# Optimization experiments

Hardware: AMD Instinct MI355X
Metric: run time of the kernel (lower is better)

Reference implementation:

```python
import jax, jax.numpy as jnp
import numpy as np

DIM = 256
NUM_HEADS = 8
KS = 3
DILATIONS = (1, 2, 3, 4)
HEAD_DIM = DIM // NUM_HEADS
SCALE = HEAD_DIM ** -0.5
HIDDEN = 4 * DIM


def setup_inputs() -> dict:
    key = jax.random.key(0)
    ks = jax.random.split(key, 8)
    B, H, W = 4, 64, 64

    def w(k, shape):
        return jax.random.normal(k, shape, jnp.float32) * 0.02

    return {
        "x": jax.random.normal(ks[0], (2, B, DIM, H, W), jnp.float32),
        "norm1_w": jnp.ones((2, DIM), jnp.float32),
        "norm1_b": jnp.zeros((2, DIM), jnp.float32),
        "q_w": w(ks[1], (2, DIM, DIM)),
        "k_w": w(ks[2], (2, DIM, DIM)),
        "v_w": w(ks[3], (2, DIM, DIM)),
        "proj_w": w(ks[4], (2, DIM, DIM)),
        "proj_b": jnp.zeros((2, DIM), jnp.float32),
        "norm2_w": jnp.ones((2, DIM), jnp.float32),
        "norm2_b": jnp.zeros((2, DIM), jnp.float32),
        "fc1_w": w(ks[5], (2, HIDDEN, DIM)),
        "fc1_b": jnp.zeros((2, HIDDEN), jnp.float32),
        "fc2_w": w(ks[6], (2, DIM, HIDDEN)),
        "fc2_b": jnp.zeros((2, DIM), jnp.float32),
    }


def _layer_norm(x, w, b, eps=1e-5):
    mu = jnp.mean(x, -1, keepdims=True)
    var = jnp.mean((x - mu) ** 2, -1, keepdims=True)
    return (x - mu) * jax.lax.rsqrt(var + eps) * w + b


def _unfold(x, ks, dil):
    # x: (B, d, H, W) -> (B, d, ks*ks, H, W); zero-padded dilated local patches
    # matches nn.Unfold(ks, dilation=dil, padding=dil*(ks-1)//2): channel-major,
    # kernel positions row-major inner.
    B, d, H, W = x.shape
    p = dil * (ks - 1) // 2
    xp = jnp.pad(x, ((0, 0), (0, 0), (p, p), (p, p)))
    pats = [xp[:, :, i * dil:i * dil + H, j * dil:j * dil + W]
            for i in range(ks) for j in range(ks)]
    return jnp.stack(pats, axis=2)


def _dilate_attn(q, k, v, dil):
    # q,k,v: (B, d, H, W) with d = DIM // num_dilation
    B, d, H, W = q.shape
    h = d // HEAD_DIM
    N = H * W
    kk = KS * KS
    qh = q.reshape(B, h, HEAD_DIM, N)                        # b h c n
    kp = _unfold(k, KS, dil).reshape(B, h, HEAD_DIM, kk, N)  # b h c k n
    attn = jnp.einsum('bhcn,bhckn->bhnk', qh, kp) * SCALE    # b h n kk
    attn = jax.nn.softmax(attn, axis=-1)
    vp = _unfold(v, KS, dil).reshape(B, h, HEAD_DIM, kk, N)
    out = jnp.einsum('bhnk,bhckn->bhnc', attn, vp)           # b h n c
    return out.transpose(0, 2, 1, 3).reshape(B, H, W, d)     # B H W d


def _mda(x1, x2, x3, qw, kw, vw, pw, pb):
    # MultiDilatelocalAttention; x*: (B, H, W, C)
    nd = len(DILATIONS)
    cd = DIM // nd
    q = jnp.einsum('bhwc,oc->bohw', x1, qw)  # 1x1 conv, no bias
    k = jnp.einsum('bhwc,oc->bohw', x2, kw)
    v = jnp.einsum('bhwc,oc->bohw', x3, vw)
    outs = [_dilate_attn(q[:, i * cd:(i + 1) * cd], k[:, i * cd:(i + 1) * cd],
                         v[:, i * cd:(i + 1) * cd], DILATIONS[i])
            for i in range(nd)]
    x = jnp.concatenate(outs, axis=-1)  # (B, H, W, C)
    return x @ pw.T + pb


def _block(x1, x2, x3, p, bi):
    # DilateBlock; inputs BCHW
    x1, x2, x3 = (t.transpose(0, 2, 3, 1) for t in (x1, x2, x3))
    n1 = lambda t: _layer_norm(t, p['norm1_w'][bi], p['norm1_b'][bi])
    x = x1 + _mda(n1(x1), n1(x2), n1(x3), p['q_w'][bi], p['k_w'][bi],
                  p['v_w'][bi], p['proj_w'][bi], p['proj_b'][bi])
    h = _layer_norm(x, p['norm2_w'][bi], p['norm2_b'][bi])
    h = jax.nn.gelu(h @ p['fc1_w'][bi].T + p['fc1_b'][bi], approximate=False)
    x = x + h @ p['fc2_w'][bi].T + p['fc2_b'][bi]
    return x.transpose(0, 3, 1, 2)


def reference(x, norm1_w, norm1_b, q_w, k_w, v_w, proj_w, proj_b,
              norm2_w, norm2_b, fc1_w, fc1_b, fc2_w, fc2_b):
    p = dict(norm1_w=norm1_w, norm1_b=norm1_b, q_w=q_w, k_w=k_w, v_w=v_w,
             proj_w=proj_w, proj_b=proj_b, norm2_w=norm2_w, norm2_b=norm2_b,
             fc1_w=fc1_w, fc1_b=fc1_b, fc2_w=fc2_w, fc2_b=fc2_b)
    vi, ir = x[0], x[1]
    vi_ir_div = _block(vi - ir, ir, ir, p, 0)
    ir_vi_div = _block(ir - vi, vi, vi, p, 1)
    return (vi_ir_div, ir_vi_div)
```

## Files before the change

### kernel.cpp

```cpp
#include <hip/hip_runtime.h>
#include <hip/hip_bf16.h>

typedef __attribute__((ext_vector_type(8))) short bf16x8;
typedef __attribute__((ext_vector_type(4))) float f32x4;

#define HWSZ 4096
#define NPIX 16384

__device__ inline float b2f(short s) {
  return __uint_as_float(((unsigned)(unsigned short)s) << 16);
}
__device__ inline short f2b(float f) {
  __hip_bfloat16 h = __float2bfloat16(f);
  return *(short*)&h;
}
__device__ inline void gl16(const short* g, short* l) {
  __builtin_amdgcn_global_load_lds(
      (const __attribute__((address_space(1))) unsigned int*)g,
      (__attribute__((address_space(3))) unsigned int*)l, 16, 0, 0);
}
__device__ inline float gelu_f(float x) {
  float ax = fabsf(x) * 0.70710678118654752f;
  float t = 1.f / (1.f + 0.3275911f * ax);
  float y = t * (0.254829592f + t * (-0.284496736f + t * (1.421413741f +
            t * (-1.453152027f + t * 1.061405429f))));
  float erfv = 1.f - y * __expf(-ax * ax);
  erfv = copysignf(erfv, x);
  return 0.5f * x * (1.f + erfv);
}

__global__ __launch_bounds__(256) void convert_k(
    const float* __restrict__ qw, const float* __restrict__ kw,
    const float* __restrict__ vw, const float* __restrict__ pw,
    const float* __restrict__ f1, const float* __restrict__ f2,
    __hip_bfloat16* __restrict__ out)
{
  int idx = blockIdx.x * 256 + threadIdx.x;
  if (idx >= 2 * 786432) return;
  int bi = idx / 786432;
  int r  = idx - bi * 786432;
  float v;
  if      (r <  65536) v = qw[bi*65536 + r];
  else if (r < 131072) v = kw[bi*65536 + r - 65536];
  else if (r < 196608) v = vw[bi*65536 + r - 131072];
  else if (r < 262144) v = pw[bi*65536 + r - 196608];
  else if (r < 524288) v = f1[bi*262144 + r - 262144];
  else                 v = f2[bi*262144 + r - 524288];
  out[idx] = __float2bfloat16(v);
}

__global__ __launch_bounds__(256) void prep2_k(
    const float* __restrict__ x,
    const float* __restrict__ nw, const float* __restrict__ nb,
    __hip_bfloat16* __restrict__ ln1a,
    __hip_bfloat16* __restrict__ ln1b,
    __hip_bfloat16* __restrict__ diff,
    float av, float ai, float bv, float bb)
{
  __shared__ float t1[16][257], t2[16][257];
  __shared__ float red[4][16][16];
  __shared__ float mu1[16], rs1[16], mu2[16], rs2[16];
  int t = threadIdx.x;
  int pix0 = blockIdx.x * 16;
  int b = pix0 >> 12, hw0 = pix0 & 4095;
  const float* vi = x + (size_t)b * 256 * HWSZ;
  const float* ir = x + (size_t)(4 + b) * 256 * HWSZ;

  for (int it = 0; it < 16; ++it) {
    int idx = it * 256 + t;
    int p = idx & 15, c = idx >> 4;
    size_t off = (size_t)c * HWSZ + hw0 + p;
    float a = vi[off], bb2 = ir[off];
    t1[p][c] = av * a + ai * bb2;
    t2[p][c] = bv * a + bb * bb2;
  }
  __syncthreads();
  {
    int p = t & 15, q = t >> 4;
    float s1 = 0, ss1 = 0, s2 = 0, ss2 = 0;
    for (int i = 0; i < 16; ++i) {
      float v = t1[p][q*16 + i]; s1 += v; ss1 += v*v;
      float u = t2[p][q*16 + i]; s2 += u; ss2 += u*u;
    }
    red[0][p][q] = s1; red[1][p][q] = ss1; red[2][p][q] = s2; red[3][p][q] = ss2;
  }
  __syncthreads();
  if (t < 32) {
    int p = t & 15, which = t >> 4;
    float s = 0, ss = 0;
    for (int q = 0; q < 16; ++q) { s += red[which*2][p][q]; ss += red[which*2+1][p][q]; }
    float mu = s * (1.f/256.f);
    float var = ss * (1.f/256.f) - mu*mu;
    float rs = rsqrtf(var + 1e-5f);
    if (which == 0) { mu1[p] = mu; rs1[p] = rs; }
    else            { mu2[p] = mu; rs2[p] = rs; }
  }
  __syncthreads();
  for (int it = 0; it < 16; ++it) {
    float v1 = t1[it][t], v2 = t2[it][t];
    size_t o = (size_t)(pix0 + it) * 256 + t;
    ln1a[o] = __float2bfloat16((v1 - mu1[it]) * rs1[it] * nw[t] + nb[t]);
    ln1b[o] = __float2bfloat16((v2 - mu2[it]) * rs2[it] * nw[t] + nb[t]);
    diff[o] = __float2bfloat16(v1);
  }
}

template<int EPI, int BN>
__device__ __forceinline__ void gemm_core(
    const short* __restrict__ A, const short* __restrict__ W,
    void* __restrict__ outp, const float* __restrict__ bias,
    const short* __restrict__ res, int K, int ldc, int m0, int n0)
{
  constexpr int NI = (BN == 128) ? 4 : 2;
  __shared__ __align__(16) short As[2][64 * 32];
  __shared__ __align__(16) short Bs[2][BN * 32];
  int tid = threadIdx.x;
  int l = tid & 63, wv = tid >> 6;
  int wm = wv >> 1, wn = wv & 1;
  int lr = l & 15, lq = l >> 4;

  int srow = tid >> 2;
  int sch = (tid & 3) ^ ((srow >> 1) & 3);
  const short* gA = A + (size_t)(m0 + srow) * K + sch * 8;
  const short* gB = W + (size_t)(n0 + srow) * K + sch * 8;
  const short* gB1 = (BN == 128) ? (W + (size_t)(n0 + srow + 64) * K + sch * 8) : nullptr;

  f32x4 acc[2][NI];
  #pragma unroll
  for (int mi = 0; mi < 2; ++mi)
    #pragma unroll
    for (int ni = 0; ni < NI; ++ni) acc[mi][ni] = (f32x4){0.f, 0.f, 0.f, 0.f};

  gl16(gA, &As[0][0] + tid * 8);
  gl16(gB, &Bs[0][0] + tid * 8);
  if constexpr (BN == 128) gl16(gB1, &Bs[0][0] + 2048 + tid * 8);
  __syncthreads();

  int cur = 0;
  int rowa0 = wm * 32 + lr;
  int rowb0 = wn * (BN / 2) + lr;
  for (int k0 = 0; k0 < K; k0 += 32) {
    int kn = k0 + 32;
    if (kn < K) {
      gl16(gA + kn, &As[cur ^ 1][0] + tid * 8);
      gl16(gB + kn, &Bs[cur ^ 1][0] + tid * 8);
      if constexpr (BN == 128) gl16(gB1 + kn, &Bs[cur ^ 1][0] + 2048 + tid * 8);
    }
    bf16x8 af[2], bfr[NI];
    #pragma unroll
    for (int mi = 0; mi < 2; ++mi) {
      int row = rowa0 + mi * 16;
      int kc = lq ^ ((row >> 1) & 3);
      af[mi] = *(const bf16x8*)(&As[cur][0] + row * 32 + kc * 8);
    }
    #pragma unroll
    for (int ni = 0; ni < NI; ++ni) {
      int row = rowb0 + ni * 16;
      int kc = lq ^ ((row >> 1) & 3);
      bfr[ni] = *(const bf16x8*)(&Bs[cur][0] + row * 32 + kc * 8);
    }
    #pragma unroll
    for (int mi = 0; mi < 2; ++mi)
      #pragma unroll
      for (int ni = 0; ni < NI; ++ni)
        acc[mi][ni] = __builtin_amdgcn_mfma_f32_16x16x32_bf16(af[mi], bfr[ni], acc[mi][ni], 0, 0, 0);
    __syncthreads();
    cur ^= 1;
  }

  #pragma unroll
  for (int mi = 0; mi < 2; ++mi)
  #pragma unroll
  for (int ni = 0; ni < NI; ++ni) {
    int row0 = m0 + wm * 32 + mi * 16 + lq * 4;
    int col = n0 + wn * (BN / 2) + ni * 16 + lr;
    if (EPI == 3) {
      float bc = bias[col];
      float4 o;
      #pragma unroll
      for (int r = 0; r < 4; ++r)
        ((float*)&o)[r] = acc[mi][ni][r] + bc + b2f(res[(size_t)(row0 + r) * 256 + col]);
      int b = row0 >> 12, hw = row0 & 4095;
      *(float4*)((float*)outp + (size_t)(b * 256 + col) * HWSZ + hw) = o;
    } else {
      #pragma unroll
      for (int r = 0; r < 4; ++r) {
        int row = row0 + r;
        float v = acc[mi][ni][r];
        if (EPI == 0) {
          ((short*)outp)[(size_t)row * ldc + col] = f2b(v);
        } else if (EPI == 1) {
          v += bias[col] + b2f(res[(size_t)row * 256 + col]);
          ((short*)outp)[(size_t)row * 256 + col] = f2b(v);
        } else {
          v = gelu_f(v + bias[col]);
          ((short*)outp)[(size_t)row * ldc + col] = f2b(v);
        }
      }
    }
  }
}

template<int EPI, int BN>
__global__ __launch_bounds__(256) void gemm6_k(
    const short* __restrict__ A, const short* __restrict__ W,
    void* __restrict__ outp, const float* __restrict__ bias,
    const short* __restrict__ res, int K, int ldc)
{
  gemm_core<EPI, BN>(A, W, outp, bias, res, K, ldc, blockIdx.x * 64, blockIdx.y * BN);
}

__global__ __launch_bounds__(256) void qkv_k(
    const short* __restrict__ ln1a, const short* __restrict__ ln1b,
    const short* __restrict__ wq, const short* __restrict__ wkv,
    short* __restrict__ qbuf, short* __restrict__ kv)
{
  bool isQ = blockIdx.y < 4;
  const short* A = isQ ? ln1a : ln1b;
  const short* W = isQ ? wq : wkv;
  void* outp = isQ ? (void*)qbuf : (void*)kv;
  int ldc = isQ ? 256 : 512;
  int n0 = (isQ ? blockIdx.y : (blockIdx.y - 4)) * 64;
  gemm_core<0, 64>(A, W, outp, nullptr, nullptr, 256, ldc, blockIdx.x * 64, n0);
}

__global__ __launch_bounds__(256) void attn2_k(
    const __hip_bfloat16* __restrict__ Q,
    const __hip_bfloat16* __restrict__ KV,
    __hip_bfloat16* __restrict__ out)
{
  int gid = blockIdx.x * 256 + threadIdx.x;
  int pix = gid >> 3, head = gid & 7;
  int dil = (head >> 1) + 1;
  int y = (pix >> 6) & 63, xc = pix & 63;
  int base = pix & ~4095;
  const short* q8 = (const short*)Q + (size_t)pix * 256 + head * 32;
  float qf[32];
  #pragma unroll
  for (int j = 0; j < 4; ++j) {
    bf16x8 v = *(const bf16x8*)(q8 + j * 8);
    #pragma unroll
    for (int e = 0; e < 8; ++e) qf[j*8 + e] = b2f(v[e]);
  }
  float lg[9];
  int npx[9];
  #pragma unroll
  for (int t = 0; t < 9; ++t) {
    int ny = y + (t / 3 - 1) * dil;
    int nx = xc + (t % 3 - 1) * dil;
    bool ok = ((unsigned)ny < 64u) && ((unsigned)nx < 64u);
    npx[t] = ok ? (base | (ny * 64 + nx)) : -1;
    float d = 0.f;
    if (ok) {
      const short* k8 = (const short*)KV + (size_t)npx[t] * 512 + head * 32;
      #pragma unroll
      for (int j = 0; j < 4; ++j) {
        bf16x8 v = *(const bf16x8*)(k8 + j * 8);
        #pragma unroll
        for (int e = 0; e < 8; ++e) d += qf[j*8 + e] * b2f(v[e]);
      }
    }
    lg[t] = d * 0.17677669529663687f;
  }
  float m = lg[0];
  #pragma unroll
  for (int t = 1; t < 9; ++t) m = fmaxf(m, lg[t]);
  float w[9], den = 0.f;
  #pragma unroll
  for (int t = 0; t < 9; ++t) { w[t] = expf(lg[t] - m); den += w[t]; }
  float inv = 1.f / den;
  float acc[32];
  #pragma unroll
  for (int j = 0; j < 32; ++j) acc[j] = 0.f;
  #pragma unroll
  for (int t = 0; t < 9; ++t) {
    if (npx[t] >= 0) {
      const short* v8 = (const short*)KV + (size_t)npx[t] * 512 + 256 + head * 32;
      float wt = w[t];
      #pragma unroll
      for (int j = 0; j < 4; ++j) {
        bf16x8 v = *(const bf16x8*)(v8 + j * 8);
        #pragma unroll
        for (int e = 0; e < 8; ++e) acc[j*8 + e] += wt * b2f(v[e]);
      }
    }
  }
  short* op = (short*)out + (size_t)pix * 256 + head * 32;
  #pragma unroll
  for (int j = 0; j < 4; ++j) {
    bf16x8 o;
    #pragma unroll
    for (int e = 0; e < 8; ++e) o[e] = f2b(acc[j*8 + e] * inv);
    *(bf16x8*)(op + j * 8) = o;
  }
}

__global__ __launch_bounds__(256) void ln2b_k(
    const __hip_bfloat16* __restrict__ xm, const float* __restrict__ w2,
    const float* __restrict__ b2, __hip_bfloat16* __restrict__ h)
{
  int pix = blockIdx.x * 4 + (threadIdx.x >> 6);
  int l = threadIdx.x & 63;
  const short* p = (const short*)xm + (size_t)pix * 256 + l * 4;
  short4 sv = *(const short4*)p;
  float vv[4] = {b2f(sv.x), b2f(sv.y), b2f(sv.z), b2f(sv.w)};
  float s = vv[0] + vv[1] + vv[2] + vv[3];
  float ss = vv[0]*vv[0] + vv[1]*vv[1] + vv[2]*vv[2] + vv[3]*vv[3];
  #pragma unroll
  for (int off = 32; off; off >>= 1) { s += __shfl_xor(s, off); ss += __shfl_xor(ss, off); }
  float mu = s * (1.f/256.f);
  float rstd = rsqrtf(ss * (1.f/256.f) - mu*mu + 1e-5f);
  #pragma unroll
  for (int j = 0; j < 4; ++j) {
    int c = l * 4 + j;
    h[(size_t)pix * 256 + c] = __float2bfloat16((vv[j] - mu) * rstd * w2[c] + b2[c]);
  }
}

extern "C" void kernel_launch(void* const* d_in, const int* in_sizes, int n_in,
                              void* d_out, int out_size, void* d_ws, size_t ws_size,
                              hipStream_t stream)
{
  const float* x   = (const float*)d_in[0];
  const float* n1w = (const float*)d_in[1];
  const float* n1b = (const float*)d_in[2];
  const float* qw  = (const float*)d_in[3];
  const float* kw  = (const float*)d_in[4];
  const float* vw  = (const float*)d_in[5];
  const float* pw  = (const float*)d_in[6];
  const float* pb  = (const float*)d_in[7];
  const float* n2w = (const float*)d_in[8];
  const float* n2b = (const float*)d_in[9];
  const float* f1w = (const float*)d_in[10];
  const float* f1b = (const float*)d_in[11];
  const float* f2w = (const float*)d_in[12];
  const float* f2b = (const float*)d_in[13];
  float* outp = (float*)d_out;
  char* ws = (char*)d_ws;

  const size_t MB = 1024 * 1024;
  __hip_bfloat16* wbf   = (__hip_bfloat16*)(ws);
  __hip_bfloat16* ln1a  = (__hip_bfloat16*)(ws + 3*MB);
  __hip_bfloat16* attnb = (__hip_bfloat16*)(ws + 3*MB);
  __hip_bfloat16* h     = (__hip_bfloat16*)(ws + 3*MB);
  __hip_bfloat16* ln1b  = (__hip_bfloat16*)(ws + 11*MB);
  __hip_bfloat16* diff  = (__hip_bfloat16*)(ws + 19*MB);
  __hip_bfloat16* qbuf  = (__hip_bfloat16*)(ws + 27*MB);
  __hip_bfloat16* kv    = (__hip_bfloat16*)(ws + 35*MB);
  __hip_bfloat16* xmid  = (__hip_bfloat16*)(ws + 35*MB);
  __hip_bfloat16* hb    = (__hip_bfloat16*)(ws + 43*MB);

  convert_k<<<6144, 256, 0, stream>>>(qw, kw, vw, pw, f1w, f2w, wbf);

  for (int bi = 0; bi < 2; ++bi) {
    const short* wq  = (const short*)(wbf + (size_t)bi * 786432);
    const short* wkv = wq + 65536;
    const short* wp  = wq + 196608;
    const short* w1  = wq + 262144;
    const short* w2  = wq + 524288;
    float av = (bi == 0) ? 1.f : -1.f, ai = (bi == 0) ? -1.f : 1.f;
    float bv = (bi == 0) ? 0.f : 1.f,  bb = (bi == 0) ? 1.f : 0.f;

    prep2_k<<<1024, 256, 0, stream>>>(x, n1w + bi*256, n1b + bi*256, ln1a, ln1b, diff, av, ai, bv, bb);

    qkv_k<<<dim3(256, 12), 256, 0, stream>>>(
        (const short*)ln1a, (const short*)ln1b, wq, wkv, (short*)qbuf, (short*)kv);

    attn2_k<<<512, 256, 0, stream>>>(qbuf, kv, attnb);

    gemm6_k<1, 64><<<dim3(256, 4), 256, 0, stream>>>(
        (const short*)attnb, wp, xmid, pb + bi*256, (const short*)diff, 256, 256);
    ln2b_k<<<4096, 256, 0, stream>>>(xmid, n2w + bi*256, n2b + bi*256, hb);

    gemm6_k<2, 128><<<dim3(256, 8), 256, 0, stream>>>(
        (const short*)hb, w1, h, f1b + bi*1024, nullptr, 256, 1024);
    gemm6_k<3, 64><<<dim3(256, 4), 256, 0, stream>>>(
        (const short*)h, w2, outp + (size_t)bi * 4194304, f2b + bi*256, (const short*)xmid, 1024, 256);
  }
}
```

Before: 233.8 us.

## Deepen GEMM global-to-LDS pipeline to 4 buffers with prefetch distance 2

Replaces the double-buffered LDS staging in the shared GEMM core with a 4-slot ring, prefetching two K-tiles ahead. Explicit vmcnt waits plus one barrier per iteration replace the trailing __syncthreads, so more global loads stay in flight while MFMAs run. The cost is doubled LDS use per block, which may reduce occupancy, and hand-written waitcnt counts that must match the number of loads issued per tile.

```diff
diff --git a/kernel.cpp b/kernel.cpp
--- a/kernel.cpp
+++ b/kernel.cpp
@@ -18,6 +18,13 @@
   __builtin_amdgcn_global_load_lds(
       (const __attribute__((address_space(1))) unsigned int*)g,
       (__attribute__((address_space(3))) unsigned int*)l, 16, 0, 0);
+}
+template<int N> __device__ __forceinline__ void vmwait() {
+  if constexpr (N == 0)      asm volatile("s_waitcnt vmcnt(0)" ::: "memory");
+  else if constexpr (N == 2) asm volatile("s_waitcnt vmcnt(2)" ::: "memory");
+  else if constexpr (N == 3) asm volatile("s_waitcnt vmcnt(3)" ::: "memory");
+  else if constexpr (N == 4) asm volatile("s_waitcnt vmcnt(4)" ::: "memory");
+  else                       asm volatile("s_waitcnt vmcnt(6)" ::: "memory");
 }
 __device__ inline float gelu_f(float x) {
   float ax = fabsf(x) * 0.70710678118654752f;
@@ -112,8 +119,9 @@
     const short* __restrict__ res, int K, int ldc, int m0, int n0)
 {
   constexpr int NI = (BN == 128) ? 4 : 2;
-  __shared__ __align__(16) short As[2][64 * 32];
-  __shared__ __align__(16) short Bs[2][BN * 32];
+  constexpr int IPT = (BN == 128) ? 3 : 2;
+  __shared__ __align__(16) short As[4][64 * 32];
+  __shared__ __align__(16) short Bs[4][BN * 32];
   int tid = threadIdx.x;
   int l = tid & 63, wv = tid >> 6;
   int wm = wv >> 1, wn = wv & 1;
@@ -131,41 +139,48 @@
     #pragma unroll
     for (int ni = 0; ni < NI; ++ni) acc[mi][ni] = (f32x4){0.f, 0.f, 0.f, 0.f};
 
-  gl16(gA, &As[0][0] + tid * 8);
-  gl16(gB, &Bs[0][0] + tid * 8);
-  if constexpr (BN == 128) gl16(gB1, &Bs[0][0] + 2048 + tid * 8);
-  __syncthreads();
-
-  int cur = 0;
+  int T = K >> 5;
+
+  #pragma unroll
+  for (int t0 = 0; t0 < 2; ++t0) {
+    gl16(gA + t0 * 32, &As[t0][0] + tid * 8);
+    gl16(gB + t0 * 32, &Bs[t0][0] + tid * 8);
+    if constexpr (BN == 128) gl16(gB1 + t0 * 32, &Bs[t0][0] + 2048 + tid * 8);
+  }
+
   int rowa0 = wm * 32 + lr;
   int rowb0 = wn * (BN / 2) + lr;
-  for (int k0 = 0; k0 < K; k0 += 32) {
-    int kn = k0 + 32;
-    if (kn < K) {
-      gl16(gA + kn, &As[cur ^ 1][0] + tid * 8);
-      gl16(gB + kn, &Bs[cur ^ 1][0] + tid * 8);
-      if constexpr (BN == 128) gl16(gB1 + kn, &Bs[cur ^ 1][0] + 2048 + tid * 8);
-    }
+  for (int t = 0; t < T; ++t) {
+    if (t + 2 < T) {
+      int b = (t + 2) & 3;
+      gl16(gA + (t + 2) * 32, &As[b][0] + tid * 8);
+      gl16(gB + (t + 2) * 32, &Bs[b][0] + tid * 8);
+      if constexpr (BN == 128) gl16(gB1 + (t + 2) * 32, &Bs[b][0] + 2048 + tid * 8);
+    }
+    if (t < T - 2)      vmwait<2 * IPT>();
+    else if (t == T - 2) vmwait<IPT>();
+    else                 vmwait<0>();
+    __builtin_amdgcn_s_barrier();
+
+    int cb = t & 3;
     bf16x8 af[2], bfr[NI];
     #pragma unroll
     for (int mi = 0; mi < 2; ++mi) {
       int row = rowa0 + mi * 16;
       int kc = lq ^ ((row >> 1) & 3);
-      af[mi] = *(const bf16x8*)(&As[cur][0] + row * 32 + kc * 8);
+      af[mi] = *(const bf16x8*)(&As[cb][0] + row * 32 + kc * 8);
     }
     #pragma unroll
     for (int ni = 0; ni < NI; ++ni) {
       int row = rowb0 + ni * 16;
       int kc = lq ^ ((row >> 1) & 3);
-      bfr[ni] = *(const bf16x8*)(&Bs[cur][0] + row * 32 + kc * 8);
+      bfr[ni] = *(const bf16x8*)(&Bs[cb][0] + row * 32 + kc * 8);
     }
     #pragma unroll
     for (int mi = 0; mi < 2; ++mi)
       #pragma unroll
       for (int ni = 0; ni < NI; ++ni)
         acc[mi][ni] = __builtin_amdgcn_mfma_f32_16x16x32_bf16(af[mi], bfr[ni], acc[mi][ni], 0, 0, 0);
-    __syncthreads();
-    cur ^= 1;
   }
 
   #pragma unroll
```

New measurement: 235.3 us. No clear change (+0.7%).
